# Kernel optimization log

Measured on AMD Instinct MI355X. Metric: run time of the kernel, lower is better.

The kernel has to match this reference:

```python
import jax, jax.numpy as jnp
import numpy as np

NEG_SLOPE = 0.2

def gat_layer(x, src, dst, W, b, a_src, a_dst, heads, out_dim, concat):
    N = x.shape[0]
    h = (x @ W).reshape(N, heads, out_dim)            # [N,H,D]
    s_src = jnp.sum(h * a_src, axis=-1)               # [N,H]
    s_dst = jnp.sum(h * a_dst, axis=-1)               # [N,H]
    e = jax.nn.leaky_relu(s_src[src] + s_dst[dst], NEG_SLOPE)  # [E,H]
    # segment softmax over destination nodes (self-loops guarantee nonempty segments)
    m = jax.ops.segment_max(e, dst, num_segments=N)
    e = jnp.exp(e - m[dst])
    denom = jax.ops.segment_sum(e, dst, num_segments=N)
    alpha = e / denom[dst]                            # [E,H]
    msg = h[src] * alpha[:, :, None]                  # [E,H,D]
    out = jax.ops.segment_sum(msg, dst, num_segments=N)  # [N,H,D]
    if concat:
        out = out.reshape(N, heads * out_dim)
    else:
        out = out.mean(axis=1)
    return out + b

def setup_inputs() -> dict:
    key = jax.random.key(0)
    ks = jax.random.split(key, 16)
    N, E = 50000, 1600000
    IN, HID, OUT, H = 128, 256, 32, 4
    D = HID // H
    def glorot(k, shape):
        fan = shape[0] + shape[-1]
        return jax.random.uniform(k, shape, jnp.float32, -1.0, 1.0) * np.sqrt(6.0 / fan)
    x = jax.random.normal(ks[0], (N, IN), jnp.float32)
    edge_index = jax.random.randint(ks[1], (2, E), 0, N, jnp.int32)
    return {
        "x": x, "edge_index": edge_index,
        "W0": glorot(ks[2], (IN, H * D)), "b0": jnp.zeros((H * D,), jnp.float32),
        "asrc0": glorot(ks[3], (H, D)), "adst0": glorot(ks[4], (H, D)),
        "W1": glorot(ks[5], (HID, H * D)), "b1": jnp.zeros((H * D,), jnp.float32),
        "asrc1": glorot(ks[6], (H, D)), "adst1": glorot(ks[7], (H, D)),
        "W2": glorot(ks[8], (HID, 1 * OUT)), "b2": jnp.zeros((OUT,), jnp.float32),
        "asrc2": glorot(ks[9], (1, OUT)), "adst2": glorot(ks[10], (1, OUT)),
    }

def reference(x, edge_index, W0, b0, asrc0, adst0, W1, b1, asrc1, adst1, W2, b2, asrc2, adst2):
    N = x.shape[0]
    # add self-loops (PyG GATConv default)
    loop = jnp.arange(N, dtype=edge_index.dtype)
    src = jnp.concatenate([edge_index[0], loop])
    dst = jnp.concatenate([edge_index[1], loop])
    h = gat_layer(x, src, dst, W0, b0, asrc0, adst0, heads=4, out_dim=64, concat=True)
    h = jax.nn.elu(h)
    h = gat_layer(h, src, dst, W1, b1, asrc1, adst1, heads=4, out_dim=64, concat=True)
    h = jax.nn.elu(h)
    h = gat_layer(h, src, dst, W2, b2, asrc2, adst2, heads=1, out_dim=32, concat=False)
    return jax.nn.log_softmax(h, axis=1)
```

## Files before the change

### kernel.cpp

```cpp
#include <hip/hip_runtime.h>
#include <hip/hip_bf16.h>
#include <math.h>

#define IN_DIM 128
#define HID    256
#define OUTD   32
#define HEADS  4
#define NB_SH  7
#define BUCKET_CAP 6144
#define NCHUNK_BLKS 256

typedef __attribute__((ext_vector_type(8))) short s8v;
typedef __attribute__((ext_vector_type(4))) float f4v;

__device__ inline unsigned short f2bf(float f) {
    union { __hip_bfloat16 b; unsigned short u; } cv;
    cv.b = __float2bfloat16(f);
    return cv.u;
}


__global__ __launch_bounds__(256) void csr_hist(const int* __restrict__ ei,
                                                int* __restrict__ H,
                                                int E, int N, int NB, int per_blk) {
    __shared__ int hist[512];
    int t = threadIdx.x;
    for (int i = t; i < NB; i += 256) hist[i] = 0;
    __syncthreads();
    int lo = blockIdx.x * per_blk;
    int hi = min(lo + per_blk, E + N);
    for (int e = lo + t; e < hi; e += 256) {
        int dst = (e < E) ? ei[E + e] : (e - E);
        atomicAdd(&hist[dst >> NB_SH], 1);
    }
    __syncthreads();
    for (int i = t; i < NB; i += 256) H[blockIdx.x * NB + i] = hist[i];
}

__global__ __launch_bounds__(256) void csr_colscan(int* __restrict__ H,
                                                   int* __restrict__ total, int NB) {
    int b = blockIdx.x, t = threadIdx.x;
    int v = H[t * NB + b];
    __shared__ int s[256];
    s[t] = v;
    __syncthreads();
    for (int o = 1; o < 256; o <<= 1) {
        int x = (t >= o) ? s[t - o] : 0;
        __syncthreads();
        s[t] += x;
        __syncthreads();
    }
    H[t * NB + b] = s[t] - v;
    if (t == 255) total[b] = s[255];
}

__global__ void csr_basescan(const int* __restrict__ total, int* __restrict__ base, int NB) {
    __shared__ int s[512];
    int t = threadIdx.x;
    int v = (t < NB) ? total[t] : 0;
    s[t] = v;
    __syncthreads();
    for (int o = 1; o < 512; o <<= 1) {
        int x = (t >= o) ? s[t - o] : 0;
        __syncthreads();
        s[t] += x;
        __syncthreads();
    }
    if (t < NB) base[t] = s[t] - v;
    if (t == NB - 1) base[NB] = s[t];
}

__global__ __launch_bounds__(256) void csr_partition(const int* __restrict__ ei,
                                                     const int* __restrict__ H,
                                                     const int* __restrict__ base,
                                                     int* __restrict__ ebuf,
                                                     int E, int N, int per_blk, int NB) {
    __shared__ int cur[512];
    int t = threadIdx.x;
    for (int i = t; i < NB; i += 256) cur[i] = base[i] + H[blockIdx.x * NB + i];
    __syncthreads();
    int lo = blockIdx.x * per_blk;
    int hi = min(lo + per_blk, E + N);
    for (int e = lo + t; e < hi; e += 256) {
        int src = (e < E) ? ei[e] : (e - E);
        int dst = (e < E) ? ei[E + e] : (e - E);
        int pos = atomicAdd(&cur[dst >> NB_SH], 1);
        ebuf[pos] = src | ((dst & 127) << 16);
    }
}

__global__ __launch_bounds__(256) void csr_sort(const int* __restrict__ ebuf,
                                                const int* __restrict__ base,
                                                int* __restrict__ col,
                                                int* __restrict__ rp, int N, int NB) {
    int b = blockIdx.x, t = threadIdx.x;
    int lo = base[b], hi = base[b + 1];
    int nbase = b << NB_SH;
    __shared__ int c_[128], sc[128], cur[128];
    __shared__ int loc[BUCKET_CAP];
    if (t < 128) c_[t] = 0;
    __syncthreads();
    for (int k = lo + t; k < hi; k += 256) atomicAdd(&c_[(ebuf[k] >> 16) & 127], 1);
    __syncthreads();
    if (t < 128) sc[t] = c_[t];
    __syncthreads();
    for (int o = 1; o < 128; o <<= 1) {
        int x = 0;
        if (t < 128 && t >= o) x = sc[t - o];
        __syncthreads();
        if (t < 128) sc[t] += x;
        __syncthreads();
    }
    if (t < 128) {
        int excl = sc[t] - c_[t];
        cur[t] = excl;
        int node = nbase + t;
        if (node < N) rp[node] = lo + excl;
    }
    if (b == NB - 1 && t == 0) rp[N] = hi;
    __syncthreads();
    for (int k = lo + t; k < hi; k += 256) {
        int e = ebuf[k];
        int p = atomicAdd(&cur[(e >> 16) & 127], 1);
        if (p < BUCKET_CAP) loc[p] = e & 0xFFFF;
    }
    __syncthreads();
    int m = min(hi - lo, BUCKET_CAP);
    for (int k = t; k < m; k += 256) col[lo + k] = loc[k];
}


__global__ __launch_bounds__(256) void prep_w(const float* __restrict__ W,
                                              unsigned short* __restrict__ Wt_h,
                                              unsigned short* __restrict__ Wt_l,
                                              int K, int N) {
    int idx = blockIdx.x * 256 + threadIdx.x;
    if (idx >= K * N) return;
    int n = idx / K, k = idx % K;
    float x = W[(size_t)k * N + n];
    unsigned short h = f2bf(x);
    float hf = __uint_as_float((unsigned)h << 16);
    Wt_h[idx] = h;
    Wt_l[idx] = f2bf(x - hf);
}

__global__ __launch_bounds__(256) void prep_x(const float* __restrict__ X,
                                              unsigned short* __restrict__ Xh,
                                              unsigned short* __restrict__ Xl,
                                              int total8) {
    int idx = blockIdx.x * 256 + threadIdx.x;
    if (idx >= total8) return;
    size_t b = (size_t)idx * 8;
    float4 v0 = *(const float4*)(X + b);
    float4 v1 = *(const float4*)(X + b + 4);
    float x[8] = {v0.x, v0.y, v0.z, v0.w, v1.x, v1.y, v1.z, v1.w};
    union { unsigned short s[8]; uint4 q; } h, l;
#pragma unroll
    for (int j = 0; j < 8; j++) {
        h.s[j] = f2bf(x[j]);
        l.s[j] = f2bf(x[j] - __uint_as_float((unsigned)h.s[j] << 16));
    }
    *(uint4*)(Xh + b) = h.q;
    *(uint4*)(Xl + b) = l.q;
}


template <int BN>
__global__ __launch_bounds__(256, 4) void gemm_mfma(const unsigned short* __restrict__ Ah,
                                                    const unsigned short* __restrict__ Al,
                                                    const unsigned short* __restrict__ Wt_h,
                                                    const unsigned short* __restrict__ Wt_l,
                                                    unsigned short* __restrict__ Cb,
                                                    const float* __restrict__ asrc,
                                                    const float* __restrict__ adst,
                                                    float* __restrict__ ssrcO,
                                                    float* __restrict__ sdstO,
                                                    int M, int K, int Nst, int Hn) {
    constexpr int WROWS = (BN == 128) ? 64 : 32;
    constexpr int WCOLS = (BN == 128) ? 64 : 32;
    constexpr int MI = WROWS / 16, NJ = WCOLS / 16;
    __shared__ unsigned short As_h[128][64], As_l[128][64];
    int tid = threadIdx.x;
    int lane = tid & 63, w = tid >> 6;
    int wm, wn;
    if (BN == 128) { wm = w & 1; wn = w >> 1; } else { wm = w; wn = 0; }
    int row0 = blockIdx.x * 128, col0 = blockIdx.y * BN;
    int lr = lane & 15;

    unsigned brow[NJ];
#pragma unroll
    for (int j = 0; j < NJ; j++)
        brow[j] = (unsigned)(col0 + wn * WCOLS + j * 16 + lr) * (unsigned)K;

    f4v acc[MI][NJ];
#pragma unroll
    for (int i = 0; i < MI; i++)
#pragma unroll
        for (int j = 0; j < NJ; j++) acc[i][j] = (f4v)(0.f);

    for (int k0 = 0; k0 < K; k0 += 64) {
#pragma unroll
        for (int i = 0; i < 4; i++) {
            int cidx = tid + i * 256;
            int r = cidx >> 3, ch = cidx & 7;
            int grow = row0 + r;
            uint4 vh = make_uint4(0, 0, 0, 0), vl = make_uint4(0, 0, 0, 0);
            if (grow < M) {
                size_t g = (size_t)grow * K + k0 + ch * 8;
                vh = *(const uint4*)(Ah + g);
                vl = *(const uint4*)(Al + g);
            }
            int chs = ch ^ (r & 7);
            *(uint4*)&As_h[r][chs * 8] = vh;
            *(uint4*)&As_l[r][chs * 8] = vl;
        }
        __syncthreads();
#pragma unroll
        for (int ks = 0; ks < 2; ks++) {
            int kc = ks * 4 + (lane >> 4);
            s8v ah[MI], al[MI], bh[NJ], bl[NJ];
            unsigned koff = (unsigned)(k0 + kc * 8);
#pragma unroll
            for (int j = 0; j < NJ; j++) {
                bh[j] = *(const s8v*)(Wt_h + brow[j] + koff);
                bl[j] = *(const s8v*)(Wt_l + brow[j] + koff);
            }
#pragma unroll
            for (int i = 0; i < MI; i++) {
                int r = wm * WROWS + i * 16 + lr;
                ah[i] = *(const s8v*)&As_h[r][(kc ^ (r & 7)) * 8];
                al[i] = *(const s8v*)&As_l[r][(kc ^ (r & 7)) * 8];
            }
#pragma unroll
            for (int i = 0; i < MI; i++)
#pragma unroll
                for (int j = 0; j < NJ; j++) {
                    acc[i][j] = __builtin_amdgcn_mfma_f32_16x16x32_bf16(ah[i], bh[j], acc[i][j], 0, 0, 0);
                    acc[i][j] = __builtin_amdgcn_mfma_f32_16x16x32_bf16(ah[i], bl[j], acc[i][j], 0, 0, 0);
                    acc[i][j] = __builtin_amdgcn_mfma_f32_16x16x32_bf16(al[i], bh[j], acc[i][j], 0, 0, 0);
                }
        }
        __syncthreads();
    }
    int lg = lane >> 4;
#pragma unroll
    for (int i = 0; i < MI; i++)
#pragma unroll
        for (int j = 0; j < NJ; j++) {
            int gcol = col0 + wn * WCOLS + j * 16 + lr;
#pragma unroll
            for (int rr = 0; rr < 4; rr++) {
                int grow = row0 + wm * WROWS + i * 16 + lg * 4 + rr;
                if (grow < M) Cb[(size_t)grow * Nst + gcol] = f2bf(acc[i][j][rr]);
            }
        }
    int hd = (BN == 128) ? (blockIdx.y * 2 + wn) : 0;
    float as_[NJ], ad_[NJ];
#pragma unroll
    for (int j = 0; j < NJ; j++) {
        int gcol = col0 + wn * WCOLS + j * 16 + lr;
        as_[j] = asrc[gcol];
        ad_[j] = adst[gcol];
    }
#pragma unroll
    for (int i = 0; i < MI; i++)
#pragma unroll
        for (int rr = 0; rr < 4; rr++) {
            float ps = 0.f, pd = 0.f;
#pragma unroll
            for (int j = 0; j < NJ; j++) {
                ps += acc[i][j][rr] * as_[j];
                pd += acc[i][j][rr] * ad_[j];
            }
#pragma unroll
            for (int off = 1; off < 16; off <<= 1) {
                ps += __shfl_xor(ps, off);
                pd += __shfl_xor(pd, off);
            }
            int grow = row0 + wm * WROWS + i * 16 + lg * 4 + rr;
            if (lr == 0 && grow < M) {
                ssrcO[(size_t)grow * Hn + hd] = ps;
                sdstO[(size_t)grow * Hn + hd] = pd;
            }
        }
}


template <int CH, int H, int MODE, int UNR>
__global__ __launch_bounds__(256) void gat_fused(const unsigned short* __restrict__ hb,
                                                 const float* __restrict__ ssrc,
                                                 const float* __restrict__ sdst,
                                                 const int* __restrict__ rp,
                                                 const int* __restrict__ col,
                                                 const float* __restrict__ bias,
                                                 float* __restrict__ outF,
                                                 unsigned short* __restrict__ outH,
                                                 unsigned short* __restrict__ outL, int N) {
    const int TPE = CH / 8;
    const int EPW = 64 / TPE;
    const int D = CH / H;
    constexpr int SHCH = (CH == 256) ? 9 : 6;
    constexpr int SHS = (H == 4) ? 4 : 2;
    int wv = threadIdx.x >> 6, lane = threadIdx.x & 63;
    int n = blockIdx.x * 4 + wv;
    if (n >= N) return;
    int k0 = __builtin_amdgcn_readfirstlane(rp[n]);
    int k1 = __builtin_amdgcn_readfirstlane(rp[n + 1]);

    int h1 = lane % H;
    int slot = lane / H;
    const int SL = 64 / H;
    float sd1 = sdst[(size_t)n * H + h1];
    float m = -1e30f, l = 0.f;
    for (int k = k0 + slot; k < k1; k += SL) {
        int s = col[k];
        float e = ssrc[(size_t)s * H + h1] + sd1;
        e = (e > 0.f) ? e : 0.2f * e;
        float mn = fmaxf(m, e);
        l = l * __expf(m - mn) + __expf(e - mn);
        m = mn;
    }
#pragma unroll
    for (int off = H; off < 64; off <<= 1) {
        float m2 = __shfl_xor(m, off);
        float l2 = __shfl_xor(l, off);
        float mn = fmaxf(m, m2);
        l = l * __expf(m - mn) + l2 * __expf(m2 - mn);
        m = mn;
    }

    int eo = lane / TPE;
    int c = (lane % TPE) * 8;
    int head = c / D;
    float mh = __shfl(m, head);
    float invl = 1.f / __shfl(l, head);
    float sdh = __shfl(sd1, head);

    const char* hbc = (const char*)hb;
    const char* ssc = (const char*)ssrc;
    unsigned cb = (unsigned)(c << 1);
    unsigned hb4 = (unsigned)(head << 2);

    float acc[8];
#pragma unroll
    for (int j = 0; j < 8; j++) acc[j] = 0.f;

    for (int k = k0; k < k1; k += UNR * EPW) {
        int ss[UNR];
        float aa[UNR];
#pragma unroll
        for (int u = 0; u < UNR; u++) {
            int ku = k + u * EPW + eo;
            bool v = ku < k1;
            ss[u] = col[v ? ku : k0];
            aa[u] = v ? invl : 0.f;
        }
        uint4 hv[UNR];
#pragma unroll
        for (int u = 0; u < UNR; u++)
            hv[u] = *(const uint4*)(hbc + (((unsigned)ss[u] << SHCH) + cb));
#pragma unroll
        for (int u = 0; u < UNR; u++) {
            float e = *(const float*)(ssc + (((unsigned)ss[u] << SHS) + hb4)) + sdh;
            e = (e > 0.f) ? e : 0.2f * e;
            aa[u] *= __expf(e - mh);
        }
#pragma unroll
        for (int u = 0; u < UNR; u++) {
            const unsigned* p = (const unsigned*)&hv[u];
#pragma unroll
            for (int q = 0; q < 4; q++) {
                acc[2 * q]     += aa[u] * __uint_as_float(p[q] << 16);
                acc[2 * q + 1] += aa[u] * __uint_as_float(p[q] & 0xffff0000u);
            }
        }
    }
#pragma unroll
    for (int off = TPE; off < 64; off <<= 1)
#pragma unroll
        for (int j = 0; j < 8; j++) acc[j] += __shfl_xor(acc[j], off);

    float o[8];
#pragma unroll
    for (int j = 0; j < 8; j++) o[j] = acc[j] + bias[c + j];
    if (MODE == 1) {
        float mx = o[0];
#pragma unroll
        for (int j = 1; j < 8; j++) mx = fmaxf(mx, o[j]);
#pragma unroll
        for (int off = 1; off < TPE; off <<= 1) mx = fmaxf(mx, __shfl_xor(mx, off));
        float sm = 0.f;
#pragma unroll
        for (int j = 0; j < 8; j++) sm += __expf(o[j] - mx);
#pragma unroll
        for (int off = 1; off < TPE; off <<= 1) sm += __shfl_xor(sm, off);
        float lg = logf(sm) + mx;
        if (eo != 0) return;
        float4* op = (float4*)(outF + (size_t)n * CH + c);
        op[0] = make_float4(o[0] - lg, o[1] - lg, o[2] - lg, o[3] - lg);
        op[1] = make_float4(o[4] - lg, o[5] - lg, o[6] - lg, o[7] - lg);
    } else {
        if (eo != 0) return;
        union { unsigned short s[8]; uint4 q; } ph, pl;
#pragma unroll
        for (int j = 0; j < 8; j++) {
            float v = (o[j] > 0.f) ? o[j] : expm1f(o[j]);
            ph.s[j] = f2bf(v);
            pl.s[j] = f2bf(v - __uint_as_float((unsigned)ph.s[j] << 16));
        }
        *(uint4*)(outH + (size_t)n * CH + c) = ph.q;
        *(uint4*)(outL + (size_t)n * CH + c) = pl.q;
    }
}


extern "C" void kernel_launch(void* const* d_in, const int* in_sizes, int n_in,
                              void* d_out, int out_size, void* d_ws, size_t ws_size,
                              hipStream_t stream) {
    const float* x   = (const float*)d_in[0];
    const int*   ei  = (const int*)d_in[1];
    const float* W0  = (const float*)d_in[2];
    const float* b0  = (const float*)d_in[3];
    const float* as0 = (const float*)d_in[4];
    const float* ad0 = (const float*)d_in[5];
    const float* W1  = (const float*)d_in[6];
    const float* b1  = (const float*)d_in[7];
    const float* as1 = (const float*)d_in[8];
    const float* ad1 = (const float*)d_in[9];
    const float* W2  = (const float*)d_in[10];
    const float* b2  = (const float*)d_in[11];
    const float* as2 = (const float*)d_in[12];
    const float* ad2 = (const float*)d_in[13];

    int N = in_sizes[0] / IN_DIM;
    int E = in_sizes[1] / 2;
    int Et = E + N;
    int NB = (N + 127) >> NB_SH;

    char* w = (char*)d_ws;
    size_t off = 0;
    auto alloc = [&](size_t bytes) -> void* {
        void* p = w + off;
        off = (off + bytes + 255) & ~(size_t)255;
        return p;
    };
    unsigned short* Qh    = (unsigned short*)alloc((size_t)N * HID * 2);
    unsigned short* Ql    = (unsigned short*)alloc((size_t)N * HID * 2);
    unsigned short* Ab    = (unsigned short*)alloc((size_t)N * HID * 2);
    unsigned short* xh    = (unsigned short*)alloc((size_t)N * IN_DIM * 2);
    unsigned short* xl    = (unsigned short*)alloc((size_t)N * IN_DIM * 2);
    float*          ssrc  = (float*)alloc((size_t)N * HEADS * 4);
    float*          sdst  = (float*)alloc((size_t)N * HEADS * 4);
    int*            rp    = (int*)alloc((size_t)(N + 1) * 4);
    int*            col   = (int*)alloc((size_t)Et * 4);
    int*            H     = (int*)alloc((size_t)NCHUNK_BLKS * NB * 4);
    int*            total = (int*)alloc((size_t)(NB + 1) * 4);
    int*            base  = (int*)alloc((size_t)(NB + 1) * 4);
    int*            ebuf  = (int*)alloc((size_t)Et * 4);
    unsigned short* Wt0h  = (unsigned short*)alloc((size_t)IN_DIM * HID * 2);
    unsigned short* Wt0l  = (unsigned short*)alloc((size_t)IN_DIM * HID * 2);
    unsigned short* Wt1h  = (unsigned short*)alloc((size_t)HID * HID * 2);
    unsigned short* Wt1l  = (unsigned short*)alloc((size_t)HID * HID * 2);
    unsigned short* Wt2h  = (unsigned short*)alloc((size_t)HID * OUTD * 2);
    unsigned short* Wt2l  = (unsigned short*)alloc((size_t)HID * OUTD * 2);

    prep_w<<<(IN_DIM * HID + 255) / 256, 256, 0, stream>>>(W0, Wt0h, Wt0l, IN_DIM, HID);
    prep_w<<<(HID * HID + 255) / 256, 256, 0, stream>>>(W1, Wt1h, Wt1l, HID, HID);
    prep_w<<<(HID * OUTD + 255) / 256, 256, 0, stream>>>(W2, Wt2h, Wt2l, HID, OUTD);
    int t8 = N * IN_DIM / 8;
    prep_x<<<(t8 + 255) / 256, 256, 0, stream>>>(x, xh, xl, t8);

    int per_blk = (Et + NCHUNK_BLKS - 1) / NCHUNK_BLKS;
    csr_hist<<<NCHUNK_BLKS, 256, 0, stream>>>(ei, H, E, N, NB, per_blk);
    csr_colscan<<<NB, 256, 0, stream>>>(H, total, NB);
    csr_basescan<<<1, 512, 0, stream>>>(total, base, NB);
    csr_partition<<<NCHUNK_BLKS, 256, 0, stream>>>(ei, H, base, ebuf, E, N, per_blk, NB);
    csr_sort<<<NB, 256, 0, stream>>>(ebuf, base, col, rp, N, NB);

    dim3 gm((N + 127) / 128, 2);
    dim3 gm2((N + 127) / 128, 1);
    int gg = (N + 3) / 4;

    gemm_mfma<128><<<gm, 256, 0, stream>>>(xh, xl, Wt0h, Wt0l, Ab, as0, ad0, ssrc, sdst,
                                           N, IN_DIM, HID, HEADS);
    gat_fused<HID, HEADS, 0, 4><<<gg, 256, 0, stream>>>(Ab, ssrc, sdst, rp, col, b0,
                                                        nullptr, Qh, Ql, N);

    gemm_mfma<128><<<gm, 256, 0, stream>>>(Qh, Ql, Wt1h, Wt1l, Ab, as1, ad1, ssrc, sdst,
                                           N, HID, HID, HEADS);
    gat_fused<HID, HEADS, 0, 4><<<gg, 256, 0, stream>>>(Ab, ssrc, sdst, rp, col, b1,
                                                        nullptr, Qh, Ql, N);

    gemm_mfma<32><<<gm2, 256, 0, stream>>>(Qh, Ql, Wt2h, Wt2l, Ab, as2, ad2, ssrc, sdst,
                                           N, HID, OUTD, 1);
    gat_fused<OUTD, 1, 1, 2><<<gg, 256, 0, stream>>>(Ab, ssrc, sdst, rp, col, b2,
                                                     (float*)d_out, nullptr, nullptr, N);
}
```

Baseline: 479.0 us.

## Stage weight tiles in LDS and halve K-step in MFMA GEMM

The GEMM now loads the transposed weight tile into shared memory alongside the activation tile, rather than having each wave read B fragments straight from global memory. The K step drops from 64 to 32 with a new XOR swizzle, and the grid is reordered so both column blocks of the same row tile launch next to each other. The launch-bounds occupancy hint goes from 4 to 2 blocks. This is meant to cut redundant global traffic for B and improve cache locality for A, at the cost of more LDS use, more barriers per K and possibly lower occupancy.

```diff
diff --git a/kernel.cpp b/kernel.cpp
--- a/kernel.cpp
+++ b/kernel.cpp
@@ -166,7 +166,7 @@
 
 
 template <int BN>
-__global__ __launch_bounds__(256, 4) void gemm_mfma(const unsigned short* __restrict__ Ah,
+__global__ __launch_bounds__(256, 2) void gemm_mfma(const unsigned short* __restrict__ Ah,
                                                     const unsigned short* __restrict__ Al,
                                                     const unsigned short* __restrict__ Wt_h,
                                                     const unsigned short* __restrict__ Wt_l,
@@ -179,30 +179,26 @@
     constexpr int WROWS = (BN == 128) ? 64 : 32;
     constexpr int WCOLS = (BN == 128) ? 64 : 32;
     constexpr int MI = WROWS / 16, NJ = WCOLS / 16;
-    __shared__ unsigned short As_h[128][64], As_l[128][64];
+    __shared__ unsigned short As_h[128][32], As_l[128][32];
+    __shared__ unsigned short Bs_h[BN][32], Bs_l[BN][32];
     int tid = threadIdx.x;
     int lane = tid & 63, w = tid >> 6;
     int wm, wn;
     if (BN == 128) { wm = w & 1; wn = w >> 1; } else { wm = w; wn = 0; }
-    int row0 = blockIdx.x * 128, col0 = blockIdx.y * BN;
+    int row0 = blockIdx.y * 128, col0 = blockIdx.x * BN;
     int lr = lane & 15;
 
-    unsigned brow[NJ];
-#pragma unroll
-    for (int j = 0; j < NJ; j++)
-        brow[j] = (unsigned)(col0 + wn * WCOLS + j * 16 + lr) * (unsigned)K;
-
     f4v acc[MI][NJ];
 #pragma unroll
     for (int i = 0; i < MI; i++)
 #pragma unroll
         for (int j = 0; j < NJ; j++) acc[i][j] = (f4v)(0.f);
 
-    for (int k0 = 0; k0 < K; k0 += 64) {
-#pragma unroll
-        for (int i = 0; i < 4; i++) {
-            int cidx = tid + i * 256;
-            int r = cidx >> 3, ch = cidx & 7;
+    for (int k0 = 0; k0 < K; k0 += 32) {
+#pragma unroll
+        for (int i = 0; i < 2; i++) {
+            int c = tid + i * 256;
+            int r = c >> 2, ch = c & 3;
             int grow = row0 + r;
             uint4 vh = make_uint4(0, 0, 0, 0), vl = make_uint4(0, 0, 0, 0);
             if (grow < M) {
@@ -210,26 +206,34 @@
                 vh = *(const uint4*)(Ah + g);
                 vl = *(const uint4*)(Al + g);
             }
-            int chs = ch ^ (r & 7);
+            int chs = ch ^ ((r >> 1) & 3);
             *(uint4*)&As_h[r][chs * 8] = vh;
             *(uint4*)&As_l[r][chs * 8] = vl;
         }
-        __syncthreads();
-#pragma unroll
-        for (int ks = 0; ks < 2; ks++) {
-            int kc = ks * 4 + (lane >> 4);
+        for (int c = tid; c < BN * 4; c += 256) {
+            int n = c >> 2, ch = c & 3;
+            int chs = ch ^ ((n >> 1) & 3);
+            size_t g = (size_t)(col0 + n) * K + k0 + ch * 8;
+            *(uint4*)&Bs_h[n][chs * 8] = *(const uint4*)(Wt_h + g);
+            *(uint4*)&Bs_l[n][chs * 8] = *(const uint4*)(Wt_l + g);
+        }
+        __syncthreads();
+        {
+            int kc = lane >> 4;
             s8v ah[MI], al[MI], bh[NJ], bl[NJ];
-            unsigned koff = (unsigned)(k0 + kc * 8);
-#pragma unroll
-            for (int j = 0; j < NJ; j++) {
-                bh[j] = *(const s8v*)(Wt_h + brow[j] + koff);
-                bl[j] = *(const s8v*)(Wt_l + brow[j] + koff);
-            }
 #pragma unroll
             for (int i = 0; i < MI; i++) {
                 int r = wm * WROWS + i * 16 + lr;
-                ah[i] = *(const s8v*)&As_h[r][(kc ^ (r & 7)) * 8];
-                al[i] = *(const s8v*)&As_l[r][(kc ^ (r & 7)) * 8];
+                int chs = kc ^ ((r >> 1) & 3);
+                ah[i] = *(const s8v*)&As_h[r][chs * 8];
+                al[i] = *(const s8v*)&As_l[r][chs * 8];
+            }
+#pragma unroll
+            for (int j = 0; j < NJ; j++) {
+                int n = wn * WCOLS + j * 16 + lr;
+                int chs = kc ^ ((n >> 1) & 3);
+                bh[j] = *(const s8v*)&Bs_h[n][chs * 8];
+                bl[j] = *(const s8v*)&Bs_l[n][chs * 8];
             }
 #pragma unroll
             for (int i = 0; i < MI; i++)
@@ -254,7 +258,7 @@
                 if (grow < M) Cb[(size_t)grow * Nst + gcol] = f2bf(acc[i][j][rr]);
             }
         }
-    int hd = (BN == 128) ? (blockIdx.y * 2 + wn) : 0;
+    int hd = (BN == 128) ? (blockIdx.x * 2 + wn) : 0;
     float as_[NJ], ad_[NJ];
 #pragma unroll
     for (int j = 0; j < NJ; j++) {
@@ -477,8 +481,8 @@
     csr_partition<<<NCHUNK_BLKS, 256, 0, stream>>>(ei, H, base, ebuf, E, N, per_blk, NB);
     csr_sort<<<NB, 256, 0, stream>>>(ebuf, base, col, rp, N, NB);
 
-    dim3 gm((N + 127) / 128, 2);
-    dim3 gm2((N + 127) / 128, 1);
+    dim3 gm(2, (N + 127) / 128);
+    dim3 gm2(1, (N + 127) / 128);
     int gg = (N + 3) / 4;
 
     gemm_mfma<128><<<gm, 256, 0, stream>>>(xh, xl, Wt0h, Wt0l, Ab, as0, ad0, ssrc, sdst,
```

New measurement: 443.1 us. 7.5% less time.
